# Optimization experiments

Hardware: AMD Instinct MI355X
Metric: run time of the kernel (lower is better)

## Reference

```python
import jax, jax.numpy as jnp
import numpy as np

EMBED_DIM = 1024
NUM_HEADS = 16
HEAD_DIM = EMBED_DIM // NUM_HEADS


def setup_inputs() -> dict:
    key = jax.random.key(0)
    k1, k2, k3, k4, k5 = jax.random.split(key, 5)
    C = EMBED_DIM
    x = jax.random.normal(k1, (4, 2048, C), dtype=jnp.float32)
    s = 1.0 / np.sqrt(C)
    qkv_w = jax.random.uniform(k2, (3 * C, C), jnp.float32, -s, s)
    qkv_b = jax.random.uniform(k3, (3 * C,), jnp.float32, -s, s)
    proj_w = jax.random.uniform(k4, (C, C), jnp.float32, -s, s)
    proj_b = jax.random.uniform(k5, (C,), jnp.float32, -s, s)
    return {"x": x, "qkv_w": qkv_w, "qkv_b": qkv_b, "proj_w": proj_w, "proj_b": proj_b}


def reference(x, qkv_w, qkv_b, proj_w, proj_b):
    B, T, C = x.shape
    H, D = NUM_HEADS, HEAD_DIM
    qkv = jnp.einsum('btc,oc->bto', x, qkv_w) + qkv_b  # [B,T,3C]
    q, k, v = jnp.split(qkv, 3, axis=2)
    # [B,T,C] -> [B,H,T,D]
    q = q.reshape(B, T, H, D).transpose(0, 2, 1, 3)
    k = k.reshape(B, T, H, D).transpose(0, 2, 1, 3)
    v = v.reshape(B, T, H, D).transpose(0, 2, 1, 3)
    scores = jnp.einsum('bhqd,bhkd->bhqk', q, k) / jnp.sqrt(jnp.float32(D)).astype(q.dtype)
    causal = jnp.tril(jnp.ones((T, T), dtype=bool))
    scores = jnp.where(causal[None, None], scores, jnp.finfo(scores.dtype).min)
    attn = jax.nn.softmax(scores, axis=-1)
    out = jnp.einsum('bhqk,bhkd->bhqd', attn, v)
    out = out.transpose(0, 2, 1, 3).reshape(B, T, C)
    return jnp.einsum('btc,oc->bto', out, proj_w) + proj_b
```

## Files before the change

kernel.cpp:

```cpp
#include <hip/hip_runtime.h>

#define EMBED 1024
#define C3    3072
#define NHEAD 16
#define HDIM  64
#define BB    4
#define TT    2048
#define MTOK  8192

typedef __bf16 bf16;
typedef __bf16 bf16x4 __attribute__((ext_vector_type(4)));
typedef __bf16 bf16x8 __attribute__((ext_vector_type(8)));
typedef float  f32x4  __attribute__((ext_vector_type(4)));
typedef float  f32x16 __attribute__((ext_vector_type(16)));
typedef unsigned int u32;

__device__ __forceinline__ void gload_lds16(const bf16* g, bf16* l) {
  __builtin_amdgcn_global_load_lds((__attribute__((address_space(1))) void*)g,
                                   (__attribute__((address_space(3))) void*)l,
                                   16, 0, 0);
}

__device__ __forceinline__ u32 pkbf(float lo, float hi_) {
  union { bf16 h[2]; u32 w; } u;
  u.h[0] = (bf16)lo; u.h[1] = (bf16)hi_;
  return u.w;
}

__global__ __launch_bounds__(256) void cvt_kernel(const float* __restrict__ in,
                                                  bf16* __restrict__ out, int n) {
  int i = (blockIdx.x * blockDim.x + threadIdx.x) * 4;
  if (i >= n) return;
  float4 v = *reinterpret_cast<const float4*>(in + i);
  bf16x4 o;
  o[0] = (bf16)v.x; o[1] = (bf16)v.y; o[2] = (bf16)v.z; o[3] = (bf16)v.w;
  *reinterpret_cast<bf16x4*>(out + i) = o;
}

__global__ __launch_bounds__(256) void gemm_qkv(const bf16* __restrict__ A,
                                                const bf16* __restrict__ W,
                                                const float* __restrict__ bias,
                                                bf16* __restrict__ Qh,
                                                bf16* __restrict__ Kh,
                                                bf16* __restrict__ VhT) {
  const int K = EMBED;
  __shared__ __align__(16) bf16 lA[128 * 32];
  __shared__ __align__(16) bf16 lB[128 * 32];
  const int tid  = threadIdx.x;
  const int lane = tid & 63;
  const int wave = tid >> 6;
  const int wm   = (wave >> 1) * 64;
  const int wn   = (wave & 1) * 64;
  const int bn0  = blockIdx.x * 128;
  const int bm0  = blockIdx.y * 128;
  const int l15  = lane & 15, lg = lane >> 4;
  const int srow = tid >> 2;
  const int sseg = tid & 3;

  f32x4 acc[4][4] = {};

  for (int kt = 0; kt < K; kt += 32) {
#pragma unroll
    for (int c = 0; c < 2; ++c) {
      int row = c * 64 + srow;
      gload_lds16(A + (size_t)(bm0 + row) * K + kt + sseg * 8, &lA[(c * 256 + tid) * 8]);
      gload_lds16(W + (size_t)(bn0 + row) * K + kt + sseg * 8, &lB[(c * 256 + tid) * 8]);
    }
    __syncthreads();
    bf16x8 af[4], bf_[4];
#pragma unroll
    for (int i = 0; i < 4; ++i)
      af[i] = *reinterpret_cast<const bf16x8*>(&lA[(wm + i * 16 + l15) * 32 + lg * 8]);
#pragma unroll
    for (int j = 0; j < 4; ++j)
      bf_[j] = *reinterpret_cast<const bf16x8*>(&lB[(wn + j * 16 + l15) * 32 + lg * 8]);
#pragma unroll
    for (int i = 0; i < 4; ++i)
#pragma unroll
      for (int j = 0; j < 4; ++j)
        acc[i][j] = __builtin_amdgcn_mfma_f32_16x16x32_bf16(af[i], bf_[j], acc[i][j], 0, 0, 0);
    __syncthreads();
  }

  const int sec = bn0 >> 10;
#pragma unroll
  for (int i = 0; i < 4; ++i)
#pragma unroll
    for (int j = 0; j < 4; ++j) {
      const int col = bn0 + wn + j * 16 + l15;
      const float bs = bias[col];
      const int c2 = col & 1023, hh = c2 >> 6, dd = c2 & 63;
      const int rowb = bm0 + wm + i * 16 + lg * 4;
      const int bb = rowb >> 11, t0 = rowb & 2047;
      const int bh = bb * 16 + hh;
      if (sec < 2) {
        bf16* dst = (sec ? Kh : Qh) + ((size_t)bh * TT + t0) * HDIM + dd;
#pragma unroll
        for (int r = 0; r < 4; ++r) dst[(size_t)r * HDIM] = (bf16)(acc[i][j][r] + bs);
      } else {
        bf16x4 o4;
#pragma unroll
        for (int r = 0; r < 4; ++r) o4[r] = (bf16)(acc[i][j][r] + bs);
        *reinterpret_cast<bf16x4*>(VhT + ((size_t)bh * HDIM + dd) * TT + t0) = o4;
      }
    }
}

__global__ __launch_bounds__(256) void gemm_bt(const bf16* __restrict__ A,
                                               const bf16* __restrict__ W,
                                               const float* __restrict__ bias,
                                               float* __restrict__ Cf,
                                               int M, int N, int K) {
  __shared__ __align__(16) bf16 lA[128 * 32];
  __shared__ __align__(16) bf16 lB[128 * 32];
  const int tid  = threadIdx.x;
  const int lane = tid & 63;
  const int wave = tid >> 6;
  const int wm   = (wave >> 1) * 64;
  const int wn   = (wave & 1) * 64;
  const int bn0  = blockIdx.x * 128;
  const int bm0  = blockIdx.y * 128;
  const int l15  = lane & 15, lg = lane >> 4;
  const int srow = tid >> 2;
  const int sseg = tid & 3;

  f32x4 acc[4][4] = {};

  for (int kt = 0; kt < K; kt += 32) {
#pragma unroll
    for (int c = 0; c < 2; ++c) {
      int row = c * 64 + srow;
      gload_lds16(A + (size_t)(bm0 + row) * K + kt + sseg * 8, &lA[(c * 256 + tid) * 8]);
      gload_lds16(W + (size_t)(bn0 + row) * K + kt + sseg * 8, &lB[(c * 256 + tid) * 8]);
    }
    __syncthreads();
    bf16x8 af[4], bf_[4];
#pragma unroll
    for (int i = 0; i < 4; ++i)
      af[i] = *reinterpret_cast<const bf16x8*>(&lA[(wm + i * 16 + l15) * 32 + lg * 8]);
#pragma unroll
    for (int j = 0; j < 4; ++j)
      bf_[j] = *reinterpret_cast<const bf16x8*>(&lB[(wn + j * 16 + l15) * 32 + lg * 8]);
#pragma unroll
    for (int i = 0; i < 4; ++i)
#pragma unroll
      for (int j = 0; j < 4; ++j)
        acc[i][j] = __builtin_amdgcn_mfma_f32_16x16x32_bf16(af[i], bf_[j], acc[i][j], 0, 0, 0);
    __syncthreads();
  }

#pragma unroll
  for (int i = 0; i < 4; ++i)
#pragma unroll
    for (int j = 0; j < 4; ++j) {
      int col = bn0 + wn + j * 16 + l15;
      float bs = bias[col];
#pragma unroll
      for (int r = 0; r < 4; ++r) {
        int row = bm0 + wm + i * 16 + lg * 4 + r;
        Cf[(size_t)row * N + col] = acc[i][j][r] + bs;
      }
    }
}

__global__ __launch_bounds__(256) void attn_kernel(const bf16* __restrict__ Qh,
                                                   const bf16* __restrict__ Kh,
                                                   const bf16* __restrict__ VhT,
                                                   bf16* __restrict__ aout) {
  __shared__ __align__(16) bf16 lK[2][64 * 64];
  __shared__ __align__(16) bf16 lVT[2][64 * 64];
  const int tid  = threadIdx.x;
  const int lane = tid & 63, wave = tid >> 6;
  const int l31  = lane & 31;
  const int hi   = lane >> 5;
  const int bh   = blockIdx.x;
  const int qt   = 15 - blockIdx.y;
  const int b    = bh >> 4, h = bh & 15;
  const int q0w  = qt * 128 + wave * 32;
  const size_t tb = (size_t)b * TT;
  const int swz  = (l31 & 7) << 4;

  const float QSCALE = 0.18033688011112042f;
  bf16x8 qfr[4];
  {
    const bf16* qrow = Qh + ((size_t)bh * TT + q0w + l31) * HDIM;
#pragma unroll
    for (int dc = 0; dc < 4; ++dc) {
      bf16x8 v = *reinterpret_cast<const bf16x8*>(qrow + dc * 16 + hi * 8);
      bf16x8 o;
#pragma unroll
      for (int j = 0; j < 8; ++j) o[j] = (bf16)((float)v[j] * QSCALE);
      qfr[dc] = o;
    }
  }

  f32x16 oacc[2] = {};
  float mrun = -3e38f, srun = 0.0f;

  const int r0 = tid >> 3, sg = tid & 7;
  const bf16* kS0 = Kh + ((size_t)bh * TT + r0) * HDIM + (size_t)(sg ^ (r0 & 7)) * 8;
  const bf16* kS1 = Kh + ((size_t)bh * TT + 32 + r0) * HDIM + (size_t)(sg ^ (r0 & 7)) * 8;
  const bf16* vS0 = VhT + ((size_t)bh * HDIM + r0) * TT + (size_t)(sg ^ (r0 & 7)) * 8;
  const bf16* vS1 = VhT + ((size_t)bh * HDIM + 32 + r0) * TT + (size_t)(sg ^ (r0 & 7)) * 8;

  const int nkv = 2 * qt + 2;

  gload_lds16(kS0, &lK[0][tid * 8]);
  gload_lds16(kS1, &lK[0][(tid + 256) * 8]);
  gload_lds16(vS0, &lVT[0][tid * 8]);
  gload_lds16(vS1, &lVT[0][(tid + 256) * 8]);
  __syncthreads();

  int cur = 0;
  for (int t = 0; t < nkv; ++t) {
    const int kv0 = t * 64;
    if (t + 1 < nkv) {
      const int kvn = kv0 + 64;
      gload_lds16(kS0 + (size_t)kvn * HDIM, &lK[cur ^ 1][tid * 8]);
      gload_lds16(kS1 + (size_t)kvn * HDIM, &lK[cur ^ 1][(tid + 256) * 8]);
      gload_lds16(vS0 + kvn, &lVT[cur ^ 1][tid * 8]);
      gload_lds16(vS1 + kvn, &lVT[cur ^ 1][(tid + 256) * 8]);
    }

    if (kv0 <= q0w + 31) {
      const char* kbase = (const char*)&lK[cur][0];
      const char* vbase = (const char*)&lVT[cur][0];

      f32x16 s0 = {}, s1 = {};
      __builtin_amdgcn_s_setprio(1);
#pragma unroll
      for (int dc = 0; dc < 4; ++dc) {
        bf16x8 kf = *reinterpret_cast<const bf16x8*>(
            kbase + l31 * 128 + (((2 * dc + hi) * 16) ^ swz));
        s0 = __builtin_amdgcn_mfma_f32_32x32x16_bf16(kf, qfr[dc], s0, 0, 0, 0);
      }
#pragma unroll
      for (int dc = 0; dc < 4; ++dc) {
        bf16x8 kf = *reinterpret_cast<const bf16x8*>(
            kbase + (32 + l31) * 128 + (((2 * dc + hi) * 16) ^ swz));
        s1 = __builtin_amdgcn_mfma_f32_32x32x16_bf16(kf, qfr[dc], s1, 0, 0, 0);
      }
      __builtin_amdgcn_s_setprio(0);

      if (kv0 + 63 > q0w) {
        const int qg = q0w + l31;
#pragma unroll
        for (int r = 0; r < 16; ++r) {
          const int kvb = kv0 + (r & 3) + 8 * (r >> 2) + 4 * hi;
          if (kvb > qg)      s0[r] = -3e38f;
          if (kvb + 32 > qg) s1[r] = -3e38f;
        }
      }

      float m8[8];
#pragma unroll
      for (int i = 0; i < 8; ++i)
        m8[i] = fmaxf(fmaxf(s0[i], s0[i + 8]), fmaxf(s1[i], s1[i + 8]));
#pragma unroll
      for (int st = 4; st > 0; st >>= 1)
#pragma unroll
        for (int i = 0; i < st; ++i) m8[i] = fmaxf(m8[i], m8[i + st]);
      float mx = fmaxf(m8[0], __shfl_xor(m8[0], 32));
      const float mnew = fmaxf(mrun, mx);
      const float corr = __builtin_amdgcn_exp2f(mrun - mnew);
      mrun = mnew;

      float psum = 0.0f;
#pragma unroll
      for (int r = 0; r < 16; ++r) {
        s0[r] = __builtin_amdgcn_exp2f(s0[r] - mnew);
        s1[r] = __builtin_amdgcn_exp2f(s1[r] - mnew);
        psum += s0[r] + s1[r];
      }
      srun = srun * corr + psum;
#pragma unroll
      for (int r = 0; r < 16; ++r) { oacc[0][r] *= corr; oacc[1][r] *= corr; }

      union { u32 w[4]; bf16x8 v; } pw[4];
#pragma unroll
      for (int cl = 0; cl < 2; ++cl) {
        {
          u32 a01 = pkbf(s0[8 * cl + 0], s0[8 * cl + 1]);
          u32 a23 = pkbf(s0[8 * cl + 2], s0[8 * cl + 3]);
          u32 b01 = pkbf(s0[8 * cl + 4], s0[8 * cl + 5]);
          u32 b23 = pkbf(s0[8 * cl + 6], s0[8 * cl + 7]);
          asm("v_permlane32_swap_b32 %0, %1" : "+v"(a01), "+v"(b01));
          asm("v_permlane32_swap_b32 %0, %1" : "+v"(a23), "+v"(b23));
          pw[cl].w[0] = a01; pw[cl].w[1] = a23; pw[cl].w[2] = b01; pw[cl].w[3] = b23;
        }
        {
          u32 a01 = pkbf(s1[8 * cl + 0], s1[8 * cl + 1]);
          u32 a23 = pkbf(s1[8 * cl + 2], s1[8 * cl + 3]);
          u32 b01 = pkbf(s1[8 * cl + 4], s1[8 * cl + 5]);
          u32 b23 = pkbf(s1[8 * cl + 6], s1[8 * cl + 7]);
          asm("v_permlane32_swap_b32 %0, %1" : "+v"(a01), "+v"(b01));
          asm("v_permlane32_swap_b32 %0, %1" : "+v"(a23), "+v"(b23));
          pw[2 + cl].w[0] = a01; pw[2 + cl].w[1] = a23; pw[2 + cl].w[2] = b01; pw[2 + cl].w[3] = b23;
        }
      }

      __builtin_amdgcn_s_setprio(1);
#pragma unroll
      for (int dh = 0; dh < 2; ++dh) {
        const char* vrow = vbase + (32 * dh + l31) * 128;
#pragma unroll
        for (int c = 0; c < 4; ++c) {
          bf16x8 vf = *reinterpret_cast<const bf16x8*>(vrow + (((2 * c + hi) * 16) ^ swz));
          oacc[dh] = __builtin_amdgcn_mfma_f32_32x32x16_bf16(vf, pw[c].v, oacc[dh], 0, 0, 0);
        }
      }
      __builtin_amdgcn_s_setprio(0);
    }
    __syncthreads();
    cur ^= 1;
  }

  srun += __shfl_xor(srun, 32);
  const float inv = 1.0f / srun;
  const int q = q0w + l31;
  bf16* orow = aout + (tb + q) * (size_t)EMBED + h * HDIM;
#pragma unroll
  for (int dh = 0; dh < 2; ++dh)
#pragma unroll
    for (int rb = 0; rb < 4; ++rb) {
      bf16x4 o4;
#pragma unroll
      for (int k = 0; k < 4; ++k) o4[k] = (bf16)(oacc[dh][4 * rb + k] * inv);
      *reinterpret_cast<bf16x4*>(orow + 32 * dh + 8 * rb + 4 * hi) = o4;
    }
}

extern "C" void kernel_launch(void* const* d_in, const int* in_sizes, int n_in,
                              void* d_out, int out_size, void* d_ws, size_t ws_size,
                              hipStream_t stream) {
  const float* x      = (const float*)d_in[0];
  const float* qkv_w  = (const float*)d_in[1];
  const float* qkv_b  = (const float*)d_in[2];
  const float* proj_w = (const float*)d_in[3];
  const float* proj_b = (const float*)d_in[4];
  float* out = (float*)d_out;

  const size_t QSZ = (size_t)BB * NHEAD * TT * HDIM;
  char* ws = (char*)d_ws;
  bf16* xb    = (bf16*)ws;
  bf16* wqkv  = xb + (size_t)MTOK * EMBED;
  bf16* wproj = wqkv + (size_t)C3 * EMBED;
  bf16* Qh    = wproj + (size_t)EMBED * EMBED;
  bf16* Kh    = Qh + QSZ;
  bf16* VhT   = Kh + QSZ;
  bf16* aob   = xb;

  cvt_kernel<<<dim3((MTOK * EMBED / 4 + 255) / 256), dim3(256), 0, stream>>>(x, xb, MTOK * EMBED);
  cvt_kernel<<<dim3((C3 * EMBED / 4 + 255) / 256), dim3(256), 0, stream>>>(qkv_w, wqkv, C3 * EMBED);
  cvt_kernel<<<dim3((EMBED * EMBED / 4 + 255) / 256), dim3(256), 0, stream>>>(proj_w, wproj, EMBED * EMBED);

  gemm_qkv<<<dim3(C3 / 128, MTOK / 128), dim3(256), 0, stream>>>(xb, wqkv, qkv_b, Qh, Kh, VhT);

  attn_kernel<<<dim3(BB * NHEAD, TT / 128), dim3(256), 0, stream>>>(Qh, Kh, VhT, aob);

  gemm_bt<<<dim3(EMBED / 128, MTOK / 128), dim3(256), 0, stream>>>(
      aob, wproj, proj_b, out, MTOK, EMBED, EMBED);
}
```

Measured before the change: 190.4 us.

## Pair high and low causal query tiles per block and skip unneeded softmax rescale

Each attention block now handles two query tiles, qt=15-p and qt=p, so every block does the same causal work, and the K/V tiles loaded into LDS are shared by both bands. The grid drops from 1024 to 512 blocks, and launch bounds now ask for 2 blocks per CU. A lazy online-softmax rescale skips the correction multiply when the wave-wide new max is within 8 (log2 units) of the running max. The costs are higher register pressure from two sets of accumulators and Q fragments, and unrenormalized exponentials that can reach 2^8 before bf16 packing.

```diff
diff --git a/kernel.cpp b/kernel.cpp
--- a/kernel.cpp
+++ b/kernel.cpp
@@ -163,39 +163,143 @@
     }
 }
 
-__global__ __launch_bounds__(256) void attn_kernel(const bf16* __restrict__ Qh,
-                                                   const bf16* __restrict__ Kh,
-                                                   const bf16* __restrict__ VhT,
-                                                   bf16* __restrict__ aout) {
+__device__ __forceinline__ void attn_tile(const char* kbase, const char* vbase,
+                                          const bf16x8 (&qfr)[4], f32x16 (&oacc)[2],
+                                          float& mrun, float& srun,
+                                          const int kv0, const int q0w,
+                                          const int l31, const int hi, const int swz) {
+  f32x16 s0 = {}, s1 = {};
+  __builtin_amdgcn_s_setprio(1);
+#pragma unroll
+  for (int dc = 0; dc < 4; ++dc) {
+    bf16x8 kf = *reinterpret_cast<const bf16x8*>(
+        kbase + l31 * 128 + (((2 * dc + hi) * 16) ^ swz));
+    s0 = __builtin_amdgcn_mfma_f32_32x32x16_bf16(kf, qfr[dc], s0, 0, 0, 0);
+  }
+#pragma unroll
+  for (int dc = 0; dc < 4; ++dc) {
+    bf16x8 kf = *reinterpret_cast<const bf16x8*>(
+        kbase + (32 + l31) * 128 + (((2 * dc + hi) * 16) ^ swz));
+    s1 = __builtin_amdgcn_mfma_f32_32x32x16_bf16(kf, qfr[dc], s1, 0, 0, 0);
+  }
+  __builtin_amdgcn_s_setprio(0);
+
+  if (kv0 + 63 > q0w) {
+    const int qg = q0w + l31;
+#pragma unroll
+    for (int r = 0; r < 16; ++r) {
+      const int kvb = kv0 + (r & 3) + 8 * (r >> 2) + 4 * hi;
+      if (kvb > qg)      s0[r] = -3e38f;
+      if (kvb + 32 > qg) s1[r] = -3e38f;
+    }
+  }
+
+  float m8[8];
+#pragma unroll
+  for (int i = 0; i < 8; ++i)
+    m8[i] = fmaxf(fmaxf(s0[i], s0[i + 8]), fmaxf(s1[i], s1[i + 8]));
+#pragma unroll
+  for (int st = 4; st > 0; st >>= 1)
+#pragma unroll
+    for (int i = 0; i < st; ++i) m8[i] = fmaxf(m8[i], m8[i + st]);
+  float mx = fmaxf(m8[0], __shfl_xor(m8[0], 32));
+
+  float mref = mrun;
+  if (!__all(mx <= mrun + 8.0f)) {
+    const float mnew = fmaxf(mrun, mx);
+    const float corr = __builtin_amdgcn_exp2f(mrun - mnew);
+    mrun = mnew; mref = mnew;
+    srun *= corr;
+#pragma unroll
+    for (int r = 0; r < 16; ++r) { oacc[0][r] *= corr; oacc[1][r] *= corr; }
+  }
+
+  float psum = 0.0f;
+#pragma unroll
+  for (int r = 0; r < 16; ++r) {
+    s0[r] = __builtin_amdgcn_exp2f(s0[r] - mref);
+    s1[r] = __builtin_amdgcn_exp2f(s1[r] - mref);
+    psum += s0[r] + s1[r];
+  }
+  srun += psum;
+
+  union { u32 w[4]; bf16x8 v; } pw[4];
+#pragma unroll
+  for (int cl = 0; cl < 2; ++cl) {
+    {
+      u32 a01 = pkbf(s0[8 * cl + 0], s0[8 * cl + 1]);
+      u32 a23 = pkbf(s0[8 * cl + 2], s0[8 * cl + 3]);
+      u32 b01 = pkbf(s0[8 * cl + 4], s0[8 * cl + 5]);
+      u32 b23 = pkbf(s0[8 * cl + 6], s0[8 * cl + 7]);
+      asm("v_permlane32_swap_b32 %0, %1" : "+v"(a01), "+v"(b01));
+      asm("v_permlane32_swap_b32 %0, %1" : "+v"(a23), "+v"(b23));
+      pw[cl].w[0] = a01; pw[cl].w[1] = a23; pw[cl].w[2] = b01; pw[cl].w[3] = b23;
+    }
+    {
+      u32 a01 = pkbf(s1[8 * cl + 0], s1[8 * cl + 1]);
+      u32 a23 = pkbf(s1[8 * cl + 2], s1[8 * cl + 3]);
+      u32 b01 = pkbf(s1[8 * cl + 4], s1[8 * cl + 5]);
+      u32 b23 = pkbf(s1[8 * cl + 6], s1[8 * cl + 7]);
+      asm("v_permlane32_swap_b32 %0, %1" : "+v"(a01), "+v"(b01));
+      asm("v_permlane32_swap_b32 %0, %1" : "+v"(a23), "+v"(b23));
+      pw[2 + cl].w[0] = a01; pw[2 + cl].w[1] = a23; pw[2 + cl].w[2] = b01; pw[2 + cl].w[3] = b23;
+    }
+  }
+
+  __builtin_amdgcn_s_setprio(1);
+#pragma unroll
+  for (int dh = 0; dh < 2; ++dh) {
+    const char* vrow = vbase + (32 * dh + l31) * 128;
+#pragma unroll
+    for (int c = 0; c < 4; ++c) {
+      bf16x8 vf = *reinterpret_cast<const bf16x8*>(vrow + (((2 * c + hi) * 16) ^ swz));
+      oacc[dh] = __builtin_amdgcn_mfma_f32_32x32x16_bf16(vf, pw[c].v, oacc[dh], 0, 0, 0);
+    }
+  }
+  __builtin_amdgcn_s_setprio(0);
+}
+
+__global__ __launch_bounds__(256, 2) void attn_kernel(const bf16* __restrict__ Qh,
+                                                      const bf16* __restrict__ Kh,
+                                                      const bf16* __restrict__ VhT,
+                                                      bf16* __restrict__ aout) {
   __shared__ __align__(16) bf16 lK[2][64 * 64];
   __shared__ __align__(16) bf16 lVT[2][64 * 64];
   const int tid  = threadIdx.x;
   const int lane = tid & 63, wave = tid >> 6;
   const int l31  = lane & 31;
   const int hi   = lane >> 5;
-  const int bh   = blockIdx.x;
-  const int qt   = 15 - blockIdx.y;
+  const int bid  = blockIdx.x;
+  const int bh   = bid & 63;
+  const int p    = bid >> 6;
+  const int qtH  = 15 - p, qtL = p;
   const int b    = bh >> 4, h = bh & 15;
-  const int q0w  = qt * 128 + wave * 32;
+  const int q0H  = qtH * 128 + wave * 32;
+  const int q0L  = qtL * 128 + wave * 32;
   const size_t tb = (size_t)b * TT;
   const int swz  = (l31 & 7) << 4;
 
   const float QSCALE = 0.18033688011112042f;
-  bf16x8 qfr[4];
+  bf16x8 qfrH[4], qfrL[4];
   {
-    const bf16* qrow = Qh + ((size_t)bh * TT + q0w + l31) * HDIM;
+    const bf16* qrowH = Qh + ((size_t)bh * TT + q0H + l31) * HDIM;
+    const bf16* qrowL = Qh + ((size_t)bh * TT + q0L + l31) * HDIM;
 #pragma unroll
     for (int dc = 0; dc < 4; ++dc) {
-      bf16x8 v = *reinterpret_cast<const bf16x8*>(qrow + dc * 16 + hi * 8);
-      bf16x8 o;
-#pragma unroll
-      for (int j = 0; j < 8; ++j) o[j] = (bf16)((float)v[j] * QSCALE);
-      qfr[dc] = o;
-    }
-  }
-
-  f32x16 oacc[2] = {};
-  float mrun = -3e38f, srun = 0.0f;
+      bf16x8 vH = *reinterpret_cast<const bf16x8*>(qrowH + dc * 16 + hi * 8);
+      bf16x8 vL = *reinterpret_cast<const bf16x8*>(qrowL + dc * 16 + hi * 8);
+      bf16x8 oH, oL;
+#pragma unroll
+      for (int j = 0; j < 8; ++j) {
+        oH[j] = (bf16)((float)vH[j] * QSCALE);
+        oL[j] = (bf16)((float)vL[j] * QSCALE);
+      }
+      qfrH[dc] = oH; qfrL[dc] = oL;
+    }
+  }
+
+  f32x16 oaccH[2] = {}, oaccL[2] = {};
+  float mH = -3e38f, sH = 0.0f, mL = -3e38f, sL = 0.0f;
 
   const int r0 = tid >> 3, sg = tid & 7;
   const bf16* kS0 = Kh + ((size_t)bh * TT + r0) * HDIM + (size_t)(sg ^ (r0 & 7)) * 8;
@@ -203,7 +307,7 @@
   const bf16* vS0 = VhT + ((size_t)bh * HDIM + r0) * TT + (size_t)(sg ^ (r0 & 7)) * 8;
   const bf16* vS1 = VhT + ((size_t)bh * HDIM + 32 + r0) * TT + (size_t)(sg ^ (r0 & 7)) * 8;
 
-  const int nkv = 2 * qt + 2;
+  const int nkv = 2 * qtH + 2;
 
   gload_lds16(kS0, &lK[0][tid * 8]);
   gload_lds16(kS1, &lK[0][(tid + 256) * 8]);
@@ -222,112 +326,35 @@
       gload_lds16(vS1 + kvn, &lVT[cur ^ 1][(tid + 256) * 8]);
     }
 
-    if (kv0 <= q0w + 31) {
-      const char* kbase = (const char*)&lK[cur][0];
-      const char* vbase = (const char*)&lVT[cur][0];
-
-      f32x16 s0 = {}, s1 = {};
-      __builtin_amdgcn_s_setprio(1);
-#pragma unroll
-      for (int dc = 0; dc < 4; ++dc) {
-        bf16x8 kf = *reinterpret_cast<const bf16x8*>(
-            kbase + l31 * 128 + (((2 * dc + hi) * 16) ^ swz));
-        s0 = __builtin_amdgcn_mfma_f32_32x32x16_bf16(kf, qfr[dc], s0, 0, 0, 0);
+    const char* kbase = (const char*)&lK[cur][0];
+    const char* vbase = (const char*)&lVT[cur][0];
+    if (kv0 <= q0H + 31)
+      attn_tile(kbase, vbase, qfrH, oaccH, mH, sH, kv0, q0H, l31, hi, swz);
+    if (kv0 <= q0L + 31)
+      attn_tile(kbase, vbase, qfrL, oaccL, mL, sL, kv0, q0L, l31, hi, swz);
+
+    __syncthreads();
+    cur ^= 1;
+  }
+
+#pragma unroll
+  for (int band = 0; band < 2; ++band) {
+    const f32x16* oacc = band ? oaccL : oaccH;
+    float sr = band ? sL : sH;
+    sr += __shfl_xor(sr, 32);
+    const float inv = 1.0f / sr;
+    const int q = (band ? q0L : q0H) + l31;
+    bf16* orow = aout + (tb + q) * (size_t)EMBED + h * HDIM;
+#pragma unroll
+    for (int dh = 0; dh < 2; ++dh)
+#pragma unroll
+      for (int rb = 0; rb < 4; ++rb) {
+        bf16x4 o4;
+#pragma unroll
+        for (int k = 0; k < 4; ++k) o4[k] = (bf16)(oacc[dh][4 * rb + k] * inv);
+        *reinterpret_cast<bf16x4*>(orow + 32 * dh + 8 * rb + 4 * hi) = o4;
       }
-#pragma unroll
-      for (int dc = 0; dc < 4; ++dc) {
-        bf16x8 kf = *reinterpret_cast<const bf16x8*>(
-            kbase + (32 + l31) * 128 + (((2 * dc + hi) * 16) ^ swz));
-        s1 = __builtin_amdgcn_mfma_f32_32x32x16_bf16(kf, qfr[dc], s1, 0, 0, 0);
-      }
-      __builtin_amdgcn_s_setprio(0);
-
-      if (kv0 + 63 > q0w) {
-        const int qg = q0w + l31;
-#pragma unroll
-        for (int r = 0; r < 16; ++r) {
-          const int kvb = kv0 + (r & 3) + 8 * (r >> 2) + 4 * hi;
-          if (kvb > qg)      s0[r] = -3e38f;
-          if (kvb + 32 > qg) s1[r] = -3e38f;
-        }
-      }
-
-      float m8[8];
-#pragma unroll
-      for (int i = 0; i < 8; ++i)
-        m8[i] = fmaxf(fmaxf(s0[i], s0[i + 8]), fmaxf(s1[i], s1[i + 8]));
-#pragma unroll
-      for (int st = 4; st > 0; st >>= 1)
-#pragma unroll
-        for (int i = 0; i < st; ++i) m8[i] = fmaxf(m8[i], m8[i + st]);
-      float mx = fmaxf(m8[0], __shfl_xor(m8[0], 32));
-      const float mnew = fmaxf(mrun, mx);
-      const float corr = __builtin_amdgcn_exp2f(mrun - mnew);
-      mrun = mnew;
-
-      float psum = 0.0f;
-#pragma unroll
-      for (int r = 0; r < 16; ++r) {
-        s0[r] = __builtin_amdgcn_exp2f(s0[r] - mnew);
-        s1[r] = __builtin_amdgcn_exp2f(s1[r] - mnew);
-        psum += s0[r] + s1[r];
-      }
-      srun = srun * corr + psum;
-#pragma unroll
-      for (int r = 0; r < 16; ++r) { oacc[0][r] *= corr; oacc[1][r] *= corr; }
-
-      union { u32 w[4]; bf16x8 v; } pw[4];
-#pragma unroll
-      for (int cl = 0; cl < 2; ++cl) {
-        {
-          u32 a01 = pkbf(s0[8 * cl + 0], s0[8 * cl + 1]);
-          u32 a23 = pkbf(s0[8 * cl + 2], s0[8 * cl + 3]);
-          u32 b01 = pkbf(s0[8 * cl + 4], s0[8 * cl + 5]);
-          u32 b23 = pkbf(s0[8 * cl + 6], s0[8 * cl + 7]);
-          asm("v_permlane32_swap_b32 %0, %1" : "+v"(a01), "+v"(b01));
-          asm("v_permlane32_swap_b32 %0, %1" : "+v"(a23), "+v"(b23));
-          pw[cl].w[0] = a01; pw[cl].w[1] = a23; pw[cl].w[2] = b01; pw[cl].w[3] = b23;
-        }
-        {
-          u32 a01 = pkbf(s1[8 * cl + 0], s1[8 * cl + 1]);
-          u32 a23 = pkbf(s1[8 * cl + 2], s1[8 * cl + 3]);
-          u32 b01 = pkbf(s1[8 * cl + 4], s1[8 * cl + 5]);
-          u32 b23 = pkbf(s1[8 * cl + 6], s1[8 * cl + 7]);
-          asm("v_permlane32_swap_b32 %0, %1" : "+v"(a01), "+v"(b01));
-          asm("v_permlane32_swap_b32 %0, %1" : "+v"(a23), "+v"(b23));
-          pw[2 + cl].w[0] = a01; pw[2 + cl].w[1] = a23; pw[2 + cl].w[2] = b01; pw[2 + cl].w[3] = b23;
-        }
-      }
-
-      __builtin_amdgcn_s_setprio(1);
-#pragma unroll
-      for (int dh = 0; dh < 2; ++dh) {
-        const char* vrow = vbase + (32 * dh + l31) * 128;
-#pragma unroll
-        for (int c = 0; c < 4; ++c) {
-          bf16x8 vf = *reinterpret_cast<const bf16x8*>(vrow + (((2 * c + hi) * 16) ^ swz));
-          oacc[dh] = __builtin_amdgcn_mfma_f32_32x32x16_bf16(vf, pw[c].v, oacc[dh], 0, 0, 0);
-        }
-      }
-      __builtin_amdgcn_s_setprio(0);
-    }
-    __syncthreads();
-    cur ^= 1;
-  }
-
-  srun += __shfl_xor(srun, 32);
-  const float inv = 1.0f / srun;
-  const int q = q0w + l31;
-  bf16* orow = aout + (tb + q) * (size_t)EMBED + h * HDIM;
-#pragma unroll
-  for (int dh = 0; dh < 2; ++dh)
-#pragma unroll
-    for (int rb = 0; rb < 4; ++rb) {
-      bf16x4 o4;
-#pragma unroll
-      for (int k = 0; k < 4; ++k) o4[k] = (bf16)(oacc[dh][4 * rb + k] * inv);
-      *reinterpret_cast<bf16x4*>(orow + 32 * dh + 8 * rb + 4 * hi) = o4;
-    }
+  }
 }
 
 extern "C" void kernel_launch(void* const* d_in, const int* in_sizes, int n_in,
@@ -356,7 +383,7 @@
 
   gemm_qkv<<<dim3(C3 / 128, MTOK / 128), dim3(256), 0, stream>>>(xb, wqkv, qkv_b, Qh, Kh, VhT);
 
-  attn_kernel<<<dim3(BB * NHEAD, TT / 128), dim3(256), 0, stream>>>(Qh, Kh, VhT, aob);
+  attn_kernel<<<dim3(512), dim3(256), 0, stream>>>(Qh, Kh, VhT, aob);
 
   gemm_bt<<<dim3(EMBED / 128, MTOK / 128), dim3(256), 0, stream>>>(
       aob, wproj, proj_b, out, MTOK, EMBED, EMBED);
```

After: 177.4 us. -6.8%, faster.
